# Performance work log

Measured on AMD Instinct MI355X. Metric: run time of the kernel, lower is better.

The kernel has to match this reference:

```python
import jax, jax.numpy as jnp
import numpy as np

B, S, D, H = 4, 2048, 512, 8
DK = D // H
SCALE = 1.0 / np.sqrt(DK)


def setup_inputs() -> dict:
    key = jax.random.key(0)
    kx, kq, kk, kv = jax.random.split(key, 4)
    w_std = np.sqrt(2.0 / (D + D))  # xavier-ish scale
    return {
        "x": jax.random.normal(kx, (B, S, D), dtype=jnp.float32),
        "W_Q": jax.random.normal(kq, (D, D), dtype=jnp.float32) * w_std,
        "W_K": jax.random.normal(kk, (D, D), dtype=jnp.float32) * w_std,
        "W_V": jax.random.normal(kv, (D, D), dtype=jnp.float32) * w_std,
    }


def reference(x, W_Q, W_K, W_V):
    # torch Linear(bias=False): y = x @ W.T
    q = jnp.einsum('bsd,ed->bse', x, W_Q).reshape(B, S, H, DK).transpose(0, 2, 1, 3)
    k = jnp.einsum('bsd,ed->bse', x, W_K).reshape(B, S, H, DK).transpose(0, 2, 1, 3)
    v = jnp.einsum('bsd,ed->bse', x, W_V).reshape(B, S, H, DK).transpose(0, 2, 1, 3)
    scores = jnp.einsum('bhqd,bhkd->bhqk', q, k) * SCALE  # [B,H,S,S]
    scores_exp = jnp.exp(scores)  # faithful: no max-subtraction in original
    attn = scores_exp / (scores_exp.sum(axis=-1, keepdims=True) + 1e-8)
    context = jnp.einsum('bhqk,bhkd->bhqd', attn, v)
    return context.transpose(0, 2, 1, 3).reshape(B, S, D)
```

## Files before the change

kernel.cpp:

```cpp
#include <hip/hip_runtime.h>
#include <hip/hip_bf16.h>

#define Bsz 4
#define Ssz 2048
#define Dsz 512
#define Hsz 8
#define DKsz 64

typedef __bf16 bf16x8 __attribute__((ext_vector_type(8)));
typedef __bf16 bf16x4 __attribute__((ext_vector_type(4)));
typedef float f32x4 __attribute__((ext_vector_type(4)));

#define SWE(c, row) ((((c) ^ ((row) & 7)) * 8))

#define GLL16(g, l) __builtin_amdgcn_global_load_lds(                      \
    (const __attribute__((address_space(1))) void*)(g),                    \
    (__attribute__((address_space(3))) void*)(l), 16, 0, 0)

__global__ __launch_bounds__(256) void cvt_kernel(
    const float* __restrict__ x, const float* __restrict__ Wq,
    const float* __restrict__ Wk, const float* __restrict__ Wv,
    __bf16* __restrict__ xb, __bf16* __restrict__ Wb)
{
    const int i = blockIdx.x * 256 + threadIdx.x;
    const int XN4 = (Bsz * Ssz * Dsz) / 4;
    const float* src;
    __bf16* dst;
    int off;
    if (i < XN4) {
        src = x; dst = xb; off = i;
    } else {
        int j = i - XN4;
        int w = j >> 16;
        off = j & 65535;
        src = (w == 0) ? Wq : (w == 1) ? Wk : Wv;
        dst = Wb + (size_t)w * (Dsz * Dsz);
    }
    float4 v = ((const float4*)src)[off];
    __bf16 o[4] = {(__bf16)v.x, (__bf16)v.y, (__bf16)v.z, (__bf16)v.w};
    *(uint2*)(dst + (size_t)off * 4) = *(uint2*)o;
}

__global__ __launch_bounds__(256, 3) void qkv_kernel(
    const __bf16* __restrict__ xb, const __bf16* __restrict__ Wb,
    __bf16* __restrict__ Qo, __bf16* __restrict__ Ko, __bf16* __restrict__ Vo)
{
    __shared__ __bf16 xs[128][64];
    __shared__ __bf16 wsh[128][64];

    const int tid  = threadIdx.x;
    const int lane = tid & 63;
    const int wave = tid >> 6;
    const int quad = lane >> 4;
    const int l16  = lane & 15;
    const int wm   = (wave & 1) * 64;
    const int wn   = (wave >> 1) * 64;

    const int lin = blockIdx.x;
    const int xcd = lin & 7;
    const int idx = lin >> 3;
    const int tnw = idx % 12;
    const int tmh = idx / 12;
    const int tm  = (tmh * 8 + xcd) * 128;
    const int tn  = (tnw & 3) * 128;
    const int which = tnw >> 2;
    const bool VM = (which == 2);
    const __bf16* W = Wb + (size_t)which * (Dsz * Dsz);

    const int rl  = lane >> 3;
    const int gch = (lane & 7) ^ rl;
    const __bf16* xsrc = xb + (size_t)(tm + wave * 8 + rl) * Dsz + gch * 8;
    const __bf16* wsrc = W  + (size_t)(tn + wave * 8 + rl) * Dsz + gch * 8;

    f32x4 acc[4][4];
    #pragma unroll
    for (int i = 0; i < 4; ++i)
        #pragma unroll
        for (int j = 0; j < 4; ++j) acc[i][j] = (f32x4){0.f, 0.f, 0.f, 0.f};

    const __bf16 (*Ash)[64] = VM ? xs : wsh;
    const __bf16 (*Bsh)[64] = VM ? wsh : xs;

    for (int k0 = 0; k0 < Dsz; k0 += 64) {
        __syncthreads();
        #pragma unroll
        for (int i = 0; i < 4; ++i) {
            GLL16(xsrc + (size_t)(32 * i) * Dsz + k0, &xs[wave * 8 + 32 * i][0]);
            GLL16(wsrc + (size_t)(32 * i) * Dsz + k0, &wsh[wave * 8 + 32 * i][0]);
        }
        asm volatile("s_waitcnt vmcnt(0)" ::: "memory");
        __syncthreads();

        #pragma unroll
        for (int kk = 0; kk < 2; ++kk) {
            bf16x8 fa[4], fb[4];
            #pragma unroll
            for (int mi = 0; mi < 4; ++mi) {
                const int row = wm + mi * 16 + l16;
                fa[mi] = *(const bf16x8*)&Ash[row][SWE(kk * 4 + quad, row)];
            }
            #pragma unroll
            for (int ni = 0; ni < 4; ++ni) {
                const int row = wn + ni * 16 + l16;
                fb[ni] = *(const bf16x8*)&Bsh[row][SWE(kk * 4 + quad, row)];
            }
            #pragma unroll
            for (int mi = 0; mi < 4; ++mi)
                #pragma unroll
                for (int ni = 0; ni < 4; ++ni)
                    acc[mi][ni] = __builtin_amdgcn_mfma_f32_16x16x32_bf16(
                        fa[mi], fb[ni], acc[mi][ni], 0, 0, 0);
        }
    }

    if (!VM) {
        const float scale = (which == 0) ? 0.125f * 1.44269504088896340736f : 1.0f;
        __bf16* dst = (which == 0) ? Qo : Ko;
        #pragma unroll
        for (int mi = 0; mi < 4; ++mi) {
            const int e0 = tn + wm + mi * 16 + quad * 4;
            const int h = e0 >> 6, d0 = e0 & 63;
            #pragma unroll
            for (int ni = 0; ni < 4; ++ni) {
                const int sf = tm + wn + ni * 16 + l16;
                const int b = sf >> 11, s = sf & (Ssz - 1);
                bf16x4 p;
                #pragma unroll
                for (int r = 0; r < 4; ++r) p[r] = (__bf16)(acc[mi][ni][r] * scale);
                *(bf16x4*)&dst[((((size_t)(b * Hsz + h) * Ssz + s)) << 6) + d0] = p;
            }
        }
    } else {
        #pragma unroll
        for (int mi = 0; mi < 4; ++mi) {
            const int sf0 = tm + wm + mi * 16 + quad * 4;
            const int b = sf0 >> 11, s0 = sf0 & (Ssz - 1);
            #pragma unroll
            for (int ni = 0; ni < 4; ++ni) {
                const int e = tn + wn + ni * 16 + l16;
                const int h = e >> 6, d = e & 63;
                bf16x4 p;
                #pragma unroll
                for (int r = 0; r < 4; ++r) p[r] = (__bf16)acc[mi][ni][r];
                *(bf16x4*)&Vo[(((size_t)(b * Hsz + h) * DKsz + d) << 11) + s0] = p;
            }
        }
    }
}

__global__ __launch_bounds__(512, 2) void attn_kernel(
    const __bf16* __restrict__ Q, const __bf16* __restrict__ K,
    const __bf16* __restrict__ VT, float* __restrict__ out)
{
    __shared__ __bf16 ks[2][64][64];
    __shared__ __bf16 vs[2][64][64];
    __shared__ __bf16 ps[8][2][16][64];

    const int tid  = threadIdx.x;
    const int lane = tid & 63;
    const int wave = tid >> 6;
    const int quad = lane >> 4;
    const int l16  = lane & 15;

    const int bh = blockIdx.x;
    const int qt = blockIdx.y;
    const int b  = bh >> 3;
    const int h  = bh & 7;

    const __bf16* Qb = Q  + (size_t)bh * Ssz * DKsz;
    const __bf16* Kb = K  + (size_t)bh * Ssz * DKsz;
    const __bf16* Vb = VT + (size_t)bh * DKsz * Ssz;

    bf16x8 qf[2][2];
    #pragma unroll
    for (int qs = 0; qs < 2; ++qs) {
        const __bf16* qrow = Qb + (size_t)(qt * 256 + wave * 32 + qs * 16 + l16) * DKsz;
        qf[qs][0] = *(const bf16x8*)(qrow + quad * 8);
        qf[qs][1] = *(const bf16x8*)(qrow + 32 + quad * 8);
    }

    bf16x8 ones;
    #pragma unroll
    for (int i = 0; i < 8; ++i) ones[i] = (__bf16)1.0f;

    f32x4 oacc[2][4];
    #pragma unroll
    for (int qs = 0; qs < 2; ++qs)
        #pragma unroll
        for (int i = 0; i < 4; ++i) oacc[qs][i] = (f32x4){0.f, 0.f, 0.f, 0.f};
    f32x4 lacc[2] = {(f32x4){0.f, 0.f, 0.f, 0.f}, (f32x4){0.f, 0.f, 0.f, 0.f}};

    const int rl  = lane >> 3;
    const int gch = (lane & 7) ^ rl;

#define STAGE_KV(DST, KBASE)                                                   \
    do {                                                                       \
        const __bf16* kgs = Kb + (size_t)((KBASE) + wave * 8 + rl) * DKsz      \
                               + gch * 8;                                      \
        const __bf16* vgs = Vb + (size_t)(wave * 8 + rl) * Ssz + (KBASE)       \
                               + gch * 8;                                      \
        GLL16(kgs, &ks[DST][wave * 8][0]);                                     \
        GLL16(vgs, &vs[DST][wave * 8][0]);                                     \
    } while (0)

    STAGE_KV(0, 0);
    asm volatile("s_waitcnt vmcnt(0)\n\ts_barrier" ::: "memory");

#define ATTN_TILE(CUR, KB)                                                     \
    do {                                                                       \
        if ((KB) + 64 < Ssz) STAGE_KV((CUR) ^ 1, (KB) + 64);                   \
        bf16x8 kf[2][4], vf[2][4];                                             \
        _Pragma("unroll")                                                      \
        for (int kk = 0; kk < 2; ++kk)                                         \
            _Pragma("unroll")                                                  \
            for (int ns = 0; ns < 4; ++ns) {                                   \
                const int row = ns * 16 + l16;                                 \
                kf[kk][ns] = *(const bf16x8*)&ks[CUR][row][SWE(kk*4+quad,row)];\
                vf[kk][ns] = *(const bf16x8*)&vs[CUR][row][SWE(kk*4+quad,row)];\
            }                                                                  \
        __builtin_amdgcn_s_setprio(1);                                         \
        f32x4 st[2][4];                                                        \
        _Pragma("unroll")                                                      \
        for (int qs = 0; qs < 2; ++qs)                                         \
            _Pragma("unroll")                                                  \
            for (int ns = 0; ns < 4; ++ns) {                                   \
                f32x4 t = (f32x4){0.f, 0.f, 0.f, 0.f};                         \
                t = __builtin_amdgcn_mfma_f32_16x16x32_bf16(                   \
                        kf[0][ns], qf[qs][0], t, 0, 0, 0);                     \
                t = __builtin_amdgcn_mfma_f32_16x16x32_bf16(                   \
                        kf[1][ns], qf[qs][1], t, 0, 0, 0);                     \
                st[qs][ns] = t;                                                \
            }                                                                  \
        __builtin_amdgcn_s_setprio(0);                                         \
        _Pragma("unroll")                                                      \
        for (int qs = 0; qs < 2; ++qs)                                         \
            _Pragma("unroll")                                                  \
            for (int ns = 0; ns < 4; ++ns) {                                   \
                bf16x4 pp;                                                     \
                _Pragma("unroll")                                              \
                for (int r = 0; r < 4; ++r)                                    \
                    pp[r] = (__bf16)__builtin_amdgcn_exp2f(st[qs][ns][r]);     \
                const int c = ns * 2 + (quad >> 1);                            \
                *(bf16x4*)&ps[wave][qs][l16]                                   \
                    [((c ^ (l16 & 7)) << 3) + ((quad & 1) << 2)] = pp;         \
            }                                                                  \
        bf16x8 af[2][2];                                                       \
        af[0][0] = *(const bf16x8*)&ps[wave][0][l16][SWE(quad, l16)];          \
        af[0][1] = *(const bf16x8*)&ps[wave][0][l16][SWE(4 + quad, l16)];      \
        af[1][0] = *(const bf16x8*)&ps[wave][1][l16][SWE(quad, l16)];          \
        af[1][1] = *(const bf16x8*)&ps[wave][1][l16][SWE(4 + quad, l16)];      \
        __builtin_amdgcn_s_setprio(1);                                         \
        _Pragma("unroll")                                                      \
        for (int qs = 0; qs < 2; ++qs) {                                       \
            _Pragma("unroll")                                                  \
            for (int ns = 0; ns < 4; ++ns) {                                   \
                oacc[qs][ns] = __builtin_amdgcn_mfma_f32_16x16x32_bf16(        \
                    vf[0][ns], af[qs][0], oacc[qs][ns], 0, 0, 0);              \
                oacc[qs][ns] = __builtin_amdgcn_mfma_f32_16x16x32_bf16(        \
                    vf[1][ns], af[qs][1], oacc[qs][ns], 0, 0, 0);              \
            }                                                                  \
            lacc[qs] = __builtin_amdgcn_mfma_f32_16x16x32_bf16(                \
                ones, af[qs][0], lacc[qs], 0, 0, 0);                           \
            lacc[qs] = __builtin_amdgcn_mfma_f32_16x16x32_bf16(                \
                ones, af[qs][1], lacc[qs], 0, 0, 0);                           \
        }                                                                      \
        __builtin_amdgcn_s_setprio(0);                                         \
        asm volatile("s_waitcnt vmcnt(0) lgkmcnt(0)\n\ts_barrier"              \
                     ::: "memory");                                            \
    } while (0)

    for (int kb = 0; kb < Ssz; kb += 128) {
        ATTN_TILE(0, kb);
        ATTN_TILE(1, kb + 64);
    }

    #pragma unroll
    for (int qs = 0; qs < 2; ++qs) {
        const float linv = 1.f / (lacc[qs][0] + 1e-8f);
        const int q = qt * 256 + wave * 32 + qs * 16 + l16;
        float* obase = out + ((size_t)b * Ssz + q) * Dsz + h * DKsz;
        #pragma unroll
        for (int ns = 0; ns < 4; ++ns) {
            f32x4 o = oacc[qs][ns] * linv;
            *(f32x4*)(obase + ns * 16 + quad * 4) = o;
        }
    }
#undef ATTN_TILE
#undef STAGE_KV
}

extern "C" void kernel_launch(void* const* d_in, const int* in_sizes, int n_in,
                              void* d_out, int out_size, void* d_ws, size_t ws_size,
                              hipStream_t stream) {
    const float* x  = (const float*)d_in[0];
    const float* Wq = (const float*)d_in[1];
    const float* Wk = (const float*)d_in[2];
    const float* Wv = (const float*)d_in[3];
    float* out = (float*)d_out;

    const size_t per = (size_t)Bsz * Hsz * Ssz * DKsz;
    __bf16* Qw  = (__bf16*)d_ws;
    __bf16* Kw  = Qw + per;
    __bf16* VTw = Kw + per;
    __bf16* xb  = VTw + per;
    __bf16* Wb  = xb + per;

    cvt_kernel<<<4864, 256, 0, stream>>>(x, Wq, Wk, Wv, xb, Wb);
    qkv_kernel<<<768, 256, 0, stream>>>(xb, Wb, Qw, Kw, VTw);
    attn_kernel<<<dim3(Bsz * Hsz, Ssz / 256), 512, 0, stream>>>(Qw, Kw, VTw, out);
}
```

Baseline: 137.3 us.

## Drop LDS staging of K/V in attention; load fragments directly from global with register prefetch

The attention kernel no longer stages K and V tiles through shared memory with global_load_lds and block barriers. Each wave now reads its K and V MFMA fragments straight from global memory into registers, double-buffering K across tiles. Blocks shrink to 256 threads covering 128 queries, which doubles the grid. This removes the per-tile barriers and LDS traffic, but each wave now fetches K/V itself, so global/L2 traffic rises and register pressure grows.

```diff
diff --git a/kernel.cpp b/kernel.cpp
--- a/kernel.cpp
+++ b/kernel.cpp
@@ -148,13 +148,11 @@
     }
 }
 
-__global__ __launch_bounds__(512, 2) void attn_kernel(
+__global__ __launch_bounds__(256, 2) void attn_kernel(
     const __bf16* __restrict__ Q, const __bf16* __restrict__ K,
     const __bf16* __restrict__ VT, float* __restrict__ out)
 {
-    __shared__ __bf16 ks[2][64][64];
-    __shared__ __bf16 vs[2][64][64];
-    __shared__ __bf16 ps[8][2][16][64];
+    __shared__ __bf16 ps[4][2][16][64];
 
     const int tid  = threadIdx.x;
     const int lane = tid & 63;
@@ -174,7 +172,7 @@
     bf16x8 qf[2][2];
     #pragma unroll
     for (int qs = 0; qs < 2; ++qs) {
-        const __bf16* qrow = Qb + (size_t)(qt * 256 + wave * 32 + qs * 16 + l16) * DKsz;
+        const __bf16* qrow = Qb + (size_t)(qt * 128 + wave * 32 + qs * 16 + l16) * DKsz;
         qf[qs][0] = *(const bf16x8*)(qrow + quad * 8);
         qf[qs][1] = *(const bf16x8*)(qrow + 32 + quad * 8);
     }
@@ -190,34 +188,24 @@
         for (int i = 0; i < 4; ++i) oacc[qs][i] = (f32x4){0.f, 0.f, 0.f, 0.f};
     f32x4 lacc[2] = {(f32x4){0.f, 0.f, 0.f, 0.f}, (f32x4){0.f, 0.f, 0.f, 0.f}};
 
-    const int rl  = lane >> 3;
-    const int gch = (lane & 7) ^ rl;
-
-#define STAGE_KV(DST, KBASE)                                                   \
+#define LOAD_KF(DST, KB)                                                       \
+    _Pragma("unroll")                                                          \
+    for (int kk = 0; kk < 2; ++kk)                                             \
+        _Pragma("unroll")                                                      \
+        for (int ns = 0; ns < 4; ++ns)                                         \
+            DST[kk][ns] = *(const bf16x8*)(Kb                                  \
+                + (size_t)((KB) + ns * 16 + l16) * DKsz + (kk * 4 + quad) * 8);
+
+#define LOAD_VF(DST, KB)                                                       \
+    _Pragma("unroll")                                                          \
+    for (int kk = 0; kk < 2; ++kk)                                             \
+        _Pragma("unroll")                                                      \
+        for (int ns = 0; ns < 4; ++ns)                                         \
+            DST[kk][ns] = *(const bf16x8*)(Vb                                  \
+                + (size_t)(ns * 16 + l16) * Ssz + (KB) + (kk * 4 + quad) * 8);
+
+#define ATTN_TILE(KF, VF, PREFETCH)                                            \
     do {                                                                       \
-        const __bf16* kgs = Kb + (size_t)((KBASE) + wave * 8 + rl) * DKsz      \
-                               + gch * 8;                                      \
-        const __bf16* vgs = Vb + (size_t)(wave * 8 + rl) * Ssz + (KBASE)       \
-                               + gch * 8;                                      \
-        GLL16(kgs, &ks[DST][wave * 8][0]);                                     \
-        GLL16(vgs, &vs[DST][wave * 8][0]);                                     \
-    } while (0)
-
-    STAGE_KV(0, 0);
-    asm volatile("s_waitcnt vmcnt(0)\n\ts_barrier" ::: "memory");
-
-#define ATTN_TILE(CUR, KB)                                                     \
-    do {                                                                       \
-        if ((KB) + 64 < Ssz) STAGE_KV((CUR) ^ 1, (KB) + 64);                   \
-        bf16x8 kf[2][4], vf[2][4];                                             \
-        _Pragma("unroll")                                                      \
-        for (int kk = 0; kk < 2; ++kk)                                         \
-            _Pragma("unroll")                                                  \
-            for (int ns = 0; ns < 4; ++ns) {                                   \
-                const int row = ns * 16 + l16;                                 \
-                kf[kk][ns] = *(const bf16x8*)&ks[CUR][row][SWE(kk*4+quad,row)];\
-                vf[kk][ns] = *(const bf16x8*)&vs[CUR][row][SWE(kk*4+quad,row)];\
-            }                                                                  \
         __builtin_amdgcn_s_setprio(1);                                         \
         f32x4 st[2][4];                                                        \
         _Pragma("unroll")                                                      \
@@ -226,12 +214,13 @@
             for (int ns = 0; ns < 4; ++ns) {                                   \
                 f32x4 t = (f32x4){0.f, 0.f, 0.f, 0.f};                         \
                 t = __builtin_amdgcn_mfma_f32_16x16x32_bf16(                   \
-                        kf[0][ns], qf[qs][0], t, 0, 0, 0);                     \
+                        KF[0][ns], qf[qs][0], t, 0, 0, 0);                     \
                 t = __builtin_amdgcn_mfma_f32_16x16x32_bf16(                   \
-                        kf[1][ns], qf[qs][1], t, 0, 0, 0);                     \
+                        KF[1][ns], qf[qs][1], t, 0, 0, 0);                     \
                 st[qs][ns] = t;                                                \
             }                                                                  \
         __builtin_amdgcn_s_setprio(0);                                         \
+        PREFETCH;                                                              \
         _Pragma("unroll")                                                      \
         for (int qs = 0; qs < 2; ++qs)                                         \
             _Pragma("unroll")                                                  \
@@ -255,9 +244,9 @@
             _Pragma("unroll")                                                  \
             for (int ns = 0; ns < 4; ++ns) {                                   \
                 oacc[qs][ns] = __builtin_amdgcn_mfma_f32_16x16x32_bf16(        \
-                    vf[0][ns], af[qs][0], oacc[qs][ns], 0, 0, 0);              \
+                    VF[0][ns], af[qs][0], oacc[qs][ns], 0, 0, 0);              \
                 oacc[qs][ns] = __builtin_amdgcn_mfma_f32_16x16x32_bf16(        \
-                    vf[1][ns], af[qs][1], oacc[qs][ns], 0, 0, 0);              \
+                    VF[1][ns], af[qs][1], oacc[qs][ns], 0, 0, 0);              \
             }                                                                  \
             lacc[qs] = __builtin_amdgcn_mfma_f32_16x16x32_bf16(                \
                 ones, af[qs][0], lacc[qs], 0, 0, 0);                           \
@@ -265,19 +254,25 @@
                 ones, af[qs][1], lacc[qs], 0, 0, 0);                           \
         }                                                                      \
         __builtin_amdgcn_s_setprio(0);                                         \
-        asm volatile("s_waitcnt vmcnt(0) lgkmcnt(0)\n\ts_barrier"              \
-                     ::: "memory");                                            \
     } while (0)
 
+    bf16x8 kfA[2][4], kfB[2][4], vf[2][4];
+
+    LOAD_KF(kfA, 0);
+
     for (int kb = 0; kb < Ssz; kb += 128) {
-        ATTN_TILE(0, kb);
-        ATTN_TILE(1, kb + 64);
+        LOAD_VF(vf, kb);
+        ATTN_TILE(kfA, vf,
+                  if (kb + 64 < Ssz) LOAD_KF(kfB, kb + 64));
+        LOAD_VF(vf, kb + 64);
+        ATTN_TILE(kfB, vf,
+                  if (kb + 128 < Ssz) LOAD_KF(kfA, kb + 128));
     }
 
     #pragma unroll
     for (int qs = 0; qs < 2; ++qs) {
         const float linv = 1.f / (lacc[qs][0] + 1e-8f);
-        const int q = qt * 256 + wave * 32 + qs * 16 + l16;
+        const int q = qt * 128 + wave * 32 + qs * 16 + l16;
         float* obase = out + ((size_t)b * Ssz + q) * Dsz + h * DKsz;
         #pragma unroll
         for (int ns = 0; ns < 4; ++ns) {
@@ -286,7 +281,8 @@
         }
     }
 #undef ATTN_TILE
-#undef STAGE_KV
+#undef LOAD_KF
+#undef LOAD_VF
 }
 
 extern "C" void kernel_launch(void* const* d_in, const int* in_sizes, int n_in,
@@ -307,5 +303,5 @@
 
     cvt_kernel<<<4864, 256, 0, stream>>>(x, Wq, Wk, Wv, xb, Wb);
     qkv_kernel<<<768, 256, 0, stream>>>(xb, Wb, Qw, Kw, VTw);
-    attn_kernel<<<dim3(Bsz * Hsz, Ssz / 256), 512, 0, stream>>>(Qw, Kw, VTw, out);
+    attn_kernel<<<dim3(Bsz * Hsz, Ssz / 128), 256, 0, stream>>>(Qw, Kw, VTw, out);
 }
```

After: 209.0 us. 52.2% more time.
